# Optimization experiments

Hardware: AMD Instinct MI355X
Metric: run time of the kernel (lower is better)

Reference implementation:

```python
import jax, jax.numpy as jnp
import numpy as np

S, D = 8192, 2048      # sequence length, feature dim (input_size)
H, E, K, L = 64, 64, 2, 64  # gate hidden, expert count, top-k, expert layer_size
EPS = 1e-12            # torch F.normalize eps


def setup_inputs() -> dict:
    key = jax.random.key(0)
    ks = jax.random.split(key, 5)
    x = jax.random.normal(ks[0], (S, D), dtype=jnp.float32)
    # torch nn.Linear weights have shape [out_features, in_features]
    Wg_in = jax.random.normal(ks[1], (H, D), dtype=jnp.float32) * 0.02   # gate.input
    Wg_lin = jax.random.normal(ks[2], (E, H), dtype=jnp.float32) * 0.02  # gate.linear
    Wg_out = jax.random.normal(ks[3], (1, S), dtype=jnp.float32) * 0.02  # gate.output
    We = jax.random.normal(ks[4], (E, L, D), dtype=jnp.float32) * 0.02   # expert weight bank
    return {"x": x, "Wg_in": Wg_in, "Wg_lin": Wg_lin, "Wg_out": Wg_out, "We": We}


def reference(x, Wg_in, Wg_lin, Wg_out, We):
    # --- SparseGate (eval mode: dropout = identity) ---
    h = x @ Wg_in.T                         # [S, H]
    logits = h @ Wg_lin.T                   # [S, E]
    scores = (logits.T @ Wg_out.T)[:, 0]    # Linear(S,1) applied to [E,S] -> [E]
    topv, idx = jax.lax.top_k(scores, K)    # global top-k experts for whole input
    g = jax.nn.softmax(topv)                # softmax over the k selected logits

    # --- dispatch to k selected experts (FFNN: Linear -> normalize(-1) -> GELU) ---
    Wsel = We[idx]                          # [K, L, D]
    z = jnp.einsum('sd,kld->ksl', x, Wsel)  # [K, S, L]
    z = z / jnp.maximum(jnp.linalg.norm(z, axis=-1, keepdims=True), EPS)
    z = jax.nn.gelu(z, approximate=False)   # torch GELU default is exact erf

    # --- weighted combine: sum_k g_k * expert_k(x) ---
    return jnp.einsum('k,ksl->sl', g, z)    # [S, L]
```

## Files before the change

kernel.cpp:

```cpp
#include <hip/hip_runtime.h>
#include <hip/hip_bf16.h>
#include <math.h>

#define D_DIM 2048
#define L_DIM 64
#define E_NUM 64
#define H_DIM 64

typedef float f32x4_t __attribute__((ext_vector_type(4)));
typedef __bf16 bf16x8_t __attribute__((ext_vector_type(8)));

#define WS_UPART 0u
#define WS_U     (128u * 2048u * 4u)
#define WS_V     (WS_U + 2048u * 4u)
#define WS_META  (WS_V + 256u)
#define WS_WB    (WS_META + 64u)
#define WS_PART  (WS_WB + 128u * 2048u * 2u)


__global__ void k_upart(const float* __restrict__ x, const float* __restrict__ wout,
                        float* __restrict__ upart) {
  const int d4 = (blockIdx.x * 256 + threadIdx.x) * 4;
  const int s0 = blockIdx.y * 64;
  const float* xp = x + (size_t)s0 * D_DIM + d4;
  float4 acc = make_float4(0.f, 0.f, 0.f, 0.f);
#pragma unroll 8
  for (int i = 0; i < 64; ++i) {
    const float w = wout[s0 + i];
    const float4 xv = *reinterpret_cast<const float4*>(xp + (size_t)i * D_DIM);
    acc.x += xv.x * w; acc.y += xv.y * w; acc.z += xv.z * w; acc.w += xv.w * w;
  }
  *reinterpret_cast<float4*>(upart + (size_t)blockIdx.y * D_DIM + d4) = acc;
}

__global__ void k_ufinish(const float* __restrict__ upart, float* __restrict__ u) {
  const int d = blockIdx.x * 256 + threadIdx.x;
  float s = 0.f;
#pragma unroll 8
  for (int c = 0; c < 128; ++c) s += upart[(size_t)c * D_DIM + d];
  u[d] = s;
}

__global__ void k_v(const float* __restrict__ wg_in, const float* __restrict__ u,
                    float* __restrict__ v) {
  const int h = blockIdx.x;
  const int t = threadIdx.x;
  const float4* wr = reinterpret_cast<const float4*>(wg_in + (size_t)h * D_DIM);
  const float4* ur = reinterpret_cast<const float4*>(u);
  float s = 0.f;
#pragma unroll
  for (int i = t; i < 512; i += 256) {
    const float4 a = wr[i];
    const float4 b = ur[i];
    s += a.x * b.x + a.y * b.y + a.z * b.z + a.w * b.w;
  }
  __shared__ float red[4];
#pragma unroll
  for (int off = 32; off; off >>= 1) s += __shfl_down(s, off, 64);
  if ((t & 63) == 0) red[t >> 6] = s;
  __syncthreads();
  if (t == 0) v[h] = red[0] + red[1] + red[2] + red[3];
}

__global__ void k_gate(const float* __restrict__ wg_lin, const float* __restrict__ v,
                       int* __restrict__ sel, float* __restrict__ g) {
  __shared__ float vv[H_DIM];
  __shared__ float sc[E_NUM];
  const int t = threadIdx.x;
  vv[t] = v[t];
  __syncthreads();
  float s = 0.f;
#pragma unroll 8
  for (int hh = 0; hh < H_DIM; ++hh) s += wg_lin[t * H_DIM + hh] * vv[hh];
  sc[t] = s;
  __syncthreads();
  if (t == 0) {
    int b1 = 0; float m1 = sc[0];
    for (int e = 1; e < E_NUM; ++e) { if (sc[e] > m1) { m1 = sc[e]; b1 = e; } }
    int b2 = -1; float m2 = -3.4e38f;
    for (int e = 0; e < E_NUM; ++e) {
      if (e != b1 && sc[e] > m2) { m2 = sc[e]; b2 = e; }
    }
    const float e2 = expf(m2 - m1);
    const float g0 = 1.0f / (1.0f + e2);
    sel[0] = b1; sel[1] = b2;
    g[0] = g0; g[1] = 1.0f - g0;
  }
}

__global__ void k_wb(const float* __restrict__ we, const int* __restrict__ sel,
                     __hip_bfloat16* __restrict__ wbt) {
  const int n = blockIdx.x;
  const int e = sel[n >> 6];
  const int l = n & 63;
  const float* src = we + ((size_t)e * L_DIM + l) * D_DIM;
  const int t = threadIdx.x;
  const int d8 = t * 8;
  const int kstep = d8 >> 6;
  const int kc = (d8 >> 3) & 7;
  const float4 a = reinterpret_cast<const float4*>(src)[2 * t];
  const float4 b = reinterpret_cast<const float4*>(src)[2 * t + 1];
  union { __hip_bfloat16 h[8]; uint4 u; } pk;
  pk.h[0] = __float2bfloat16(a.x); pk.h[1] = __float2bfloat16(a.y);
  pk.h[2] = __float2bfloat16(a.z); pk.h[3] = __float2bfloat16(a.w);
  pk.h[4] = __float2bfloat16(b.x); pk.h[5] = __float2bfloat16(b.y);
  pk.h[6] = __float2bfloat16(b.z); pk.h[7] = __float2bfloat16(b.w);
  const size_t off = (size_t)kstep * 8192 + n * 64 + ((kc ^ (n & 7)) * 8);
  *reinterpret_cast<uint4*>(wbt + off) = pk.u;
}

__device__ __forceinline__ void async_ld16(const void* gp, void* lp) {
  __builtin_amdgcn_global_load_lds(
      (const __attribute__((address_space(1))) unsigned int*)gp,
      (__attribute__((address_space(3))) unsigned int*)lp, 16, 0, 0);
}

__device__ __forceinline__ float gelu_f(float v) {
  return 0.5f * v * (1.0f + erff(v * 0.70710678118654752440f));
}

__global__ __launch_bounds__(256, 4) void k_moe_gemm(
    const float* __restrict__ x, const __hip_bfloat16* __restrict__ wbt,
    float* __restrict__ part) {
  __shared__ __align__(16) unsigned char ldsA[8192];
  __shared__ __align__(16) unsigned char ldsB[2][16384];

  const int tid = threadIdx.x;
  const int w = tid >> 6, lane = tid & 63;
  const int wm = w >> 1, wn = w & 1;
  const int mb = blockIdx.x;
  const int kg = blockIdx.y;
  const int fr = lane & 15, fq = lane >> 4;
  const int m0 = mb * 64;

  const int c0 = tid, c1 = 256 + tid;
  const int r0_ = c0 >> 3, kc0 = c0 & 7, r1_ = c1 >> 3, kc1 = c1 & 7;
  unsigned char* aw0 = ldsA + r0_ * 128 + ((kc0 ^ (r0_ & 7)) << 4);
  unsigned char* aw1 = ldsA + r1_ * 128 + ((kc1 ^ (r1_ & 7)) << 4);
  const float* gA0 = x + (size_t)(m0 + r0_) * D_DIM + kc0 * 8;
  const float* gA1 = x + (size_t)(m0 + r1_) * D_DIM + kc1 * 8;

  f32x4_t acc[2][4];
#pragma unroll
  for (int mf = 0; mf < 2; ++mf)
#pragma unroll
    for (int nf = 0; nf < 4; ++nf) acc[mf][nf] = (f32x4_t){0.f, 0.f, 0.f, 0.f};

  union { __hip_bfloat16 h[8]; uint4 u; } pk;
  float4 ar[4];

  auto cvt_write = [&]() {
    pk.h[0] = __float2bfloat16(ar[0].x); pk.h[1] = __float2bfloat16(ar[0].y);
    pk.h[2] = __float2bfloat16(ar[0].z); pk.h[3] = __float2bfloat16(ar[0].w);
    pk.h[4] = __float2bfloat16(ar[1].x); pk.h[5] = __float2bfloat16(ar[1].y);
    pk.h[6] = __float2bfloat16(ar[1].z); pk.h[7] = __float2bfloat16(ar[1].w);
    *reinterpret_cast<uint4*>(aw0) = pk.u;
    pk.h[0] = __float2bfloat16(ar[2].x); pk.h[1] = __float2bfloat16(ar[2].y);
    pk.h[2] = __float2bfloat16(ar[2].z); pk.h[3] = __float2bfloat16(ar[2].w);
    pk.h[4] = __float2bfloat16(ar[3].x); pk.h[5] = __float2bfloat16(ar[3].y);
    pk.h[6] = __float2bfloat16(ar[3].z); pk.h[7] = __float2bfloat16(ar[3].w);
    *reinterpret_cast<uint4*>(aw1) = pk.u;
  };

  {
    const int k0 = (kg * 4) * 64;
    ar[0] = *reinterpret_cast<const float4*>(gA0 + k0);
    ar[1] = *reinterpret_cast<const float4*>(gA0 + k0 + 4);
    ar[2] = *reinterpret_cast<const float4*>(gA1 + k0);
    ar[3] = *reinterpret_cast<const float4*>(gA1 + k0 + 4);
#pragma unroll
    for (int ph = 0; ph < 4; ++ph) {
      const int c = ph * 256 + tid;
      async_ld16(wbt + (size_t)(kg * 4) * 8192 + c * 8, &ldsB[0][c * 16]);
    }
    cvt_write();
    __syncthreads();
  }

  for (int kk = 0; kk < 4; ++kk) {
    const int cur = kk & 1;
    union fragu { uint4 u; bf16x8_t v; };
    fragu af[2][2], bf_[4][2];
#pragma unroll
    for (int mf = 0; mf < 2; ++mf)
#pragma unroll
      for (int ks = 0; ks < 2; ++ks) {
        const int arr = wm * 32 + mf * 16 + fr;
        const int kq = ks * 4 + fq;
        af[mf][ks].u = *reinterpret_cast<const uint4*>(
            ldsA + arr * 128 + ((kq ^ (arr & 7)) * 16));
      }
#pragma unroll
    for (int nf = 0; nf < 4; ++nf)
#pragma unroll
      for (int ks = 0; ks < 2; ++ks) {
        const int br = wn * 64 + nf * 16 + fr;
        const int kq = ks * 4 + fq;
        bf_[nf][ks].u = *reinterpret_cast<const uint4*>(
            ldsB[cur] + br * 128 + ((kq ^ (br & 7)) * 16));
      }
    if (kk < 3) {
      const int k0n = (kg * 4 + kk + 1) * 64;
      ar[0] = *reinterpret_cast<const float4*>(gA0 + k0n);
      ar[1] = *reinterpret_cast<const float4*>(gA0 + k0n + 4);
      ar[2] = *reinterpret_cast<const float4*>(gA1 + k0n);
      ar[3] = *reinterpret_cast<const float4*>(gA1 + k0n + 4);
      __builtin_amdgcn_sched_barrier(0);
#pragma unroll
      for (int ph = 0; ph < 4; ++ph) {
        const int c = ph * 256 + tid;
        async_ld16(wbt + (size_t)(kg * 4 + kk + 1) * 8192 + c * 8,
                   &ldsB[cur ^ 1][c * 16]);
      }
      __builtin_amdgcn_sched_barrier(0);
    }
#pragma unroll
    for (int mf = 0; mf < 2; ++mf)
#pragma unroll
      for (int nf = 0; nf < 4; ++nf) {
        acc[mf][nf] = __builtin_amdgcn_mfma_f32_16x16x32_bf16(
            af[mf][0].v, bf_[nf][0].v, acc[mf][nf], 0, 0, 0);
        acc[mf][nf] = __builtin_amdgcn_mfma_f32_16x16x32_bf16(
            af[mf][1].v, bf_[nf][1].v, acc[mf][nf], 0, 0, 0);
      }
    asm volatile("s_waitcnt lgkmcnt(0)" ::: "memory");
    __builtin_amdgcn_s_barrier();
    __builtin_amdgcn_sched_barrier(0);
    if (kk < 3) {
      cvt_write();
    }
    asm volatile("s_waitcnt vmcnt(0) lgkmcnt(0)" ::: "memory");
    __builtin_amdgcn_s_barrier();
    __builtin_amdgcn_sched_barrier(0);
  }

#pragma unroll
  for (int mf = 0; mf < 2; ++mf)
#pragma unroll
    for (int nf = 0; nf < 4; ++nf)
#pragma unroll
      for (int reg = 0; reg < 4; ++reg) {
        const int r = m0 + wm * 32 + mf * 16 + fq * 4 + reg;
        const int c = wn * 64 + nf * 16 + fr;
        part[((size_t)kg * 8192 + r) * 128 + c] = acc[mf][nf][reg];
      }
}

__global__ __launch_bounds__(256) void k_finish(const float* __restrict__ part,
                                                const float* __restrict__ gw,
                                                float* __restrict__ out) {
  __shared__ float z[32 * 132];
  __shared__ float ps[32 * 8];
  const int tid = threadIdx.x;
  const int m0 = blockIdx.x * 32;
  const float g0 = gw[0], g1 = gw[1];
  const size_t KSTRIDE = (size_t)8192 * 128;
#pragma unroll
  for (int p = 0; p < 4; ++p) {
    const int idx = p * 256 + tid;
    const int r = idx >> 5, c4 = (idx & 31) * 4;
    const float* pp = part + ((size_t)(m0 + r)) * 128 + c4;
    f32x4_t s = (f32x4_t){0.f, 0.f, 0.f, 0.f};
#pragma unroll
    for (int kgi = 0; kgi < 8; ++kgi)
      s = s + *reinterpret_cast<const f32x4_t*>(pp + kgi * KSTRIDE);
    z[r * 132 + c4 + 0] = s[0];
    z[r * 132 + c4 + 1] = s[1];
    z[r * 132 + c4 + 2] = s[2];
    z[r * 132 + c4 + 3] = s[3];
  }
  __syncthreads();
  {
    const int r = tid >> 3, seg = tid & 7;
    float s = 0.f;
#pragma unroll
    for (int i2 = 0; i2 < 16; ++i2) {
      const float t2 = z[r * 132 + seg * 16 + i2];
      s += t2 * t2;
    }
    ps[r * 8 + seg] = s;
  }
  __syncthreads();
  {
    const int r = tid >> 3, j = tid & 7;
    const float s0 = ps[r * 8 + 0] + ps[r * 8 + 1] + ps[r * 8 + 2] + ps[r * 8 + 3];
    const float s1 = ps[r * 8 + 4] + ps[r * 8 + 5] + ps[r * 8 + 6] + ps[r * 8 + 7];
    const float i0 = 1.0f / fmaxf(sqrtf(s0), 1e-12f);
    const float i1 = 1.0f / fmaxf(sqrtf(s1), 1e-12f);
    float o[8];
#pragma unroll
    for (int i2 = 0; i2 < 8; ++i2) {
      const int c = j * 8 + i2;
      const float za = z[r * 132 + c] * i0;
      const float zb2 = z[r * 132 + 64 + c] * i1;
      o[i2] = g0 * gelu_f(za) + g1 * gelu_f(zb2);
    }
    float4* op = reinterpret_cast<float4*>(out + (size_t)(m0 + r) * 64 + j * 8);
    op[0] = make_float4(o[0], o[1], o[2], o[3]);
    op[1] = make_float4(o[4], o[5], o[6], o[7]);
  }
}

extern "C" void kernel_launch(void* const* d_in, const int* in_sizes, int n_in,
                              void* d_out, int out_size, void* d_ws, size_t ws_size,
                              hipStream_t stream) {
  (void)in_sizes; (void)n_in; (void)out_size; (void)ws_size;
  const float* x      = (const float*)d_in[0];
  const float* wg_in  = (const float*)d_in[1];
  const float* wg_lin = (const float*)d_in[2];
  const float* wg_out = (const float*)d_in[3];
  const float* we     = (const float*)d_in[4];
  float* out = (float*)d_out;
  char* ws = (char*)d_ws;

  float* upart = (float*)(ws + WS_UPART);
  float* u     = (float*)(ws + WS_U);
  float* v     = (float*)(ws + WS_V);
  int*   sel   = (int*)(ws + WS_META);
  float* g     = (float*)(ws + WS_META + 8);
  __hip_bfloat16* wbt = (__hip_bfloat16*)(ws + WS_WB);
  float* part = (float*)(ws + WS_PART);

  k_upart  <<<dim3(2, 128), 256, 0, stream>>>(x, wg_out, upart);
  k_ufinish<<<8, 256, 0, stream>>>(upart, u);
  k_v      <<<64, 256, 0, stream>>>(wg_in, u, v);
  k_gate   <<<1, 64, 0, stream>>>(wg_lin, v, sel, g);
  k_wb     <<<128, 256, 0, stream>>>(we, sel, wbt);
  k_moe_gemm<<<dim3(128, 8), 256, 0, stream>>>(x, wbt, part);
  k_finish <<<256, 256, 0, stream>>>(part, g, out);
}
```

Baseline: 159.3 us.

## Fuse gate projection into u-partial kernel and drop two launches

Each k_upart block now projects its partial u-chunk (1024 features) onto Wg_in right away. It writes a 64-wide partial v instead of a 2048-wide partial u. The k_ufinish and k_v kernels go away, and k_gate (now 256 threads) reduces the 256 partial v vectors before scoring. This removes two kernel launches and the partial-u write and read traffic. In exchange every block re-reads a 256 KB slice of Wg_in and does 64 wave reductions, and the final reduction runs in a single block.

After: 187.5 us. 17.7% more time.

```diff
diff --git a/kernel.cpp b/kernel.cpp
--- a/kernel.cpp
+++ b/kernel.cpp
@@ -10,17 +10,19 @@
 typedef float f32x4_t __attribute__((ext_vector_type(4)));
 typedef __bf16 bf16x8_t __attribute__((ext_vector_type(8)));
 
-#define WS_UPART 0u
-#define WS_U     (128u * 2048u * 4u)
-#define WS_V     (WS_U + 2048u * 4u)
-#define WS_META  (WS_V + 256u)
+#define WS_VPART 0u
+#define WS_META  (256u * 64u * 4u)
 #define WS_WB    (WS_META + 64u)
 #define WS_PART  (WS_WB + 128u * 2048u * 2u)
 
 
 __global__ void k_upart(const float* __restrict__ x, const float* __restrict__ wout,
-                        float* __restrict__ upart) {
-  const int d4 = (blockIdx.x * 256 + threadIdx.x) * 4;
+                        const float* __restrict__ wg_in, float* __restrict__ vpart) {
+  __shared__ float sacc[1024];
+  __shared__ float vred[64][4];
+  const int t = threadIdx.x;
+  const int bx = blockIdx.x;
+  const int d4 = (bx * 256 + t) * 4;
   const int s0 = blockIdx.y * 64;
   const float* xp = x + (size_t)s0 * D_DIM + d4;
   float4 acc = make_float4(0.f, 0.f, 0.f, 0.f);
@@ -30,49 +32,48 @@
     const float4 xv = *reinterpret_cast<const float4*>(xp + (size_t)i * D_DIM);
     acc.x += xv.x * w; acc.y += xv.y * w; acc.z += xv.z * w; acc.w += xv.w * w;
   }
-  *reinterpret_cast<float4*>(upart + (size_t)blockIdx.y * D_DIM + d4) = acc;
-}
-
-__global__ void k_ufinish(const float* __restrict__ upart, float* __restrict__ u) {
-  const int d = blockIdx.x * 256 + threadIdx.x;
-  float s = 0.f;
-#pragma unroll 8
-  for (int c = 0; c < 128; ++c) s += upart[(size_t)c * D_DIM + d];
-  u[d] = s;
-}
-
-__global__ void k_v(const float* __restrict__ wg_in, const float* __restrict__ u,
-                    float* __restrict__ v) {
-  const int h = blockIdx.x;
-  const int t = threadIdx.x;
-  const float4* wr = reinterpret_cast<const float4*>(wg_in + (size_t)h * D_DIM);
-  const float4* ur = reinterpret_cast<const float4*>(u);
-  float s = 0.f;
-#pragma unroll
-  for (int i = t; i < 512; i += 256) {
-    const float4 a = wr[i];
-    const float4 b = ur[i];
-    s += a.x * b.x + a.y * b.y + a.z * b.z + a.w * b.w;
-  }
-  __shared__ float red[4];
-#pragma unroll
-  for (int off = 32; off; off >>= 1) s += __shfl_down(s, off, 64);
-  if ((t & 63) == 0) red[t >> 6] = s;
-  __syncthreads();
-  if (t == 0) v[h] = red[0] + red[1] + red[2] + red[3];
-}
-
-__global__ void k_gate(const float* __restrict__ wg_lin, const float* __restrict__ v,
+  *reinterpret_cast<float4*>(&sacc[t * 4]) = acc;
+  __syncthreads();
+  const int wv = t >> 6, lane = t & 63;
+  const float4* wg4 = reinterpret_cast<const float4*>(wg_in) + bx * 256;
+  const float4* sa4 = reinterpret_cast<const float4*>(sacc);
+  const float4 b = sa4[t];
+#pragma unroll 4
+  for (int h = 0; h < 64; ++h) {
+    const float4 a = wg4[(size_t)h * 512 + t];
+    float s = a.x * b.x + a.y * b.y + a.z * b.z + a.w * b.w;
+#pragma unroll
+    for (int off = 32; off; off >>= 1) s += __shfl_down(s, off, 64);
+    if (lane == 0) vred[h][wv] = s;
+  }
+  __syncthreads();
+  if (t < 64)
+    vpart[((size_t)blockIdx.y * 2 + bx) * 64 + t] =
+        vred[t][0] + vred[t][1] + vred[t][2] + vred[t][3];
+}
+
+__global__ void k_gate(const float* __restrict__ wg_lin, const float* __restrict__ vpart,
                        int* __restrict__ sel, float* __restrict__ g) {
+  __shared__ float vq[4][H_DIM];
   __shared__ float vv[H_DIM];
   __shared__ float sc[E_NUM];
   const int t = threadIdx.x;
-  vv[t] = v[t];
-  __syncthreads();
-  float s = 0.f;
+  const int h = t & 63, q = t >> 6;
+  {
+    float s = 0.f;
 #pragma unroll 8
-  for (int hh = 0; hh < H_DIM; ++hh) s += wg_lin[t * H_DIM + hh] * vv[hh];
-  sc[t] = s;
+    for (int c = q * 64; c < q * 64 + 64; ++c) s += vpart[(size_t)c * 64 + h];
+    vq[q][h] = s;
+  }
+  __syncthreads();
+  if (t < 64) vv[t] = vq[0][t] + vq[1][t] + vq[2][t] + vq[3][t];
+  __syncthreads();
+  if (t < 64) {
+    float s = 0.f;
+#pragma unroll 8
+    for (int hh = 0; hh < H_DIM; ++hh) s += wg_lin[t * H_DIM + hh] * vv[hh];
+    sc[t] = s;
+  }
   __syncthreads();
   if (t == 0) {
     int b1 = 0; float m1 = sc[0];
@@ -313,18 +314,14 @@
   float* out = (float*)d_out;
   char* ws = (char*)d_ws;
 
-  float* upart = (float*)(ws + WS_UPART);
-  float* u     = (float*)(ws + WS_U);
-  float* v     = (float*)(ws + WS_V);
+  float* vpart = (float*)(ws + WS_VPART);
   int*   sel   = (int*)(ws + WS_META);
   float* g     = (float*)(ws + WS_META + 8);
   __hip_bfloat16* wbt = (__hip_bfloat16*)(ws + WS_WB);
   float* part = (float*)(ws + WS_PART);
 
-  k_upart  <<<dim3(2, 128), 256, 0, stream>>>(x, wg_out, upart);
-  k_ufinish<<<8, 256, 0, stream>>>(upart, u);
-  k_v      <<<64, 256, 0, stream>>>(wg_in, u, v);
-  k_gate   <<<1, 64, 0, stream>>>(wg_lin, v, sel, g);
+  k_upart  <<<dim3(2, 128), 256, 0, stream>>>(x, wg_out, wg_in, vpart);
+  k_gate   <<<1, 256, 0, stream>>>(wg_lin, vpart, sel, g);
   k_wb     <<<128, 256, 0, stream>>>(we, sel, wbt);
   k_moe_gemm<<<dim3(128, 8), 256, 0, stream>>>(x, wbt, part);
   k_finish <<<256, 256, 0, stream>>>(part, g, out);
```
